# Kernel tuning notes

Measured on AMD Instinct MI355X. Metric: run time of the kernel, lower is better.

Reference implementation:

```python
import jax, jax.numpy as jnp
import numpy as np

NODE = 112
L1, L2, L3 = 256, 128, 64
BATCH = 2048


def setup_inputs() -> dict:
    key = jax.random.key(0)
    ks = jax.random.split(key, 19)
    def n(k, shape, s=0.05):
        return jax.random.normal(k, shape, jnp.float32) * s
    return {
        "x": jax.random.uniform(ks[0], (BATCH, NODE, NODE), jnp.float32),
        # GAT1: proj Linear(112->L1); attention Linear(2*L1->1) split into (wa1, wb1, ba1)
        "Wp1": n(ks[1], (L1, NODE)), "bp1": n(ks[2], (L1,)),
        "wa1": n(ks[3], (L1,)), "wb1": n(ks[4], (L1,)), "ba1": n(ks[5], ()),
        # Pool1: proj Linear(L1->1)
        "Wpool1": n(ks[6], (L1,)), "bpool1": n(ks[7], ()),
        # GAT2
        "Wp2": n(ks[8], (L2, L1)), "bp2": n(ks[9], (L2,)),
        "wa2": n(ks[10], (L2,)), "wb2": n(ks[11], (L2,)), "ba2": n(ks[12], ()),
        # Pool2
        "Wpool2": n(ks[13], (L2,)), "bpool2": n(ks[14], ()),
        # FC head
        "Wfc1": n(ks[15], (L3, L2)), "bfc1": n(ks[16], (L3,)),
        "Wfc2": n(ks[17], (1, L3)), "bfc2": n(ks[18], (1,)),
    }


def _gat(a, h, Wp, bp, wa, wb, ba):
    # h: [B,N,Din] -> [B,N,O]
    h = jnp.einsum('bnd,od->bno', h, Wp) + bp
    # attention(concat(h_i, h_j)) == h_i.wa + h_j.wb + ba (linear over concat splits)
    s = jnp.einsum('bno,o->bn', h, wa)  # first-half contribution
    t = jnp.einsum('bno,o->bn', h, wb)  # second-half contribution
    e = jax.nn.relu(s[:, :, None] + t[:, None, :] + ba)  # [B,N,N]
    att = jnp.exp(e) * a
    att = att / jnp.sum(att, axis=-1, keepdims=True)
    return jnp.einsum('bij,bjo->bio', att, h) + h


def _pool(adj, hidden, w, b, k):
    scores = jax.nn.sigmoid(jnp.einsum('bnd,d->bn', hidden, w) + b)  # [B,N]
    vals, idx = jax.lax.top_k(scores, k)  # sorted descending, like torch.topk
    hidden = jnp.take_along_axis(hidden, idx[:, :, None], axis=1) * vals[:, :, None]
    adj = jnp.take_along_axis(adj, idx[:, :, None], axis=1)
    adj = jnp.take_along_axis(adj, idx[:, None, :], axis=2)
    adj = adj / jnp.sum(adj, axis=-1, keepdims=True)
    return adj, hidden


def reference(x, Wp1, bp1, wa1, wb1, ba1, Wpool1, bpool1,
              Wp2, bp2, wa2, wb2, ba2, Wpool2, bpool2,
              Wfc1, bfc1, Wfc2, bfc2):
    b = x.shape[0]
    h = jnp.broadcast_to(jnp.eye(NODE, dtype=x.dtype), (b, NODE, NODE))
    h = jax.nn.relu(_gat(x, h, Wp1, bp1, wa1, wb1, ba1))
    k1 = max(2, int(0.5 * NODE))          # 56
    a, h = _pool(x, h, Wpool1, bpool1, k1)
    h = jax.nn.relu(_gat(a, h, Wp2, bp2, wa2, wb2, ba2))
    k2 = max(2, int(0.5 * k1))            # 28
    a, h = _pool(a, h, Wpool2, bpool2, k2)
    h = jnp.mean(h, axis=1)               # [B,L2]
    h = jax.nn.relu(h @ Wfc1.T + bfc1)
    return h @ Wfc2.T + bfc2              # [B,1]
```

## Files before the change

kernel.cpp:

```cpp
#include <hip/hip_runtime.h>

#define NODE 112
#define KP1 56
#define KP2 28
#define D1 256
#define D2 128
#define NBATCH 2048
#define NCH 4
#define CR 28
#define WR 7

typedef const float* __restrict__ fp;

__global__ void k0a(fp Wp1, fp bp1, fp wa1, fp wb1,
                    float* __restrict__ s1, float* __restrict__ t1)
{
    int tid = threadIdx.x;
    if (tid < NODE) {
        float sa = 0.f, sb = 0.f;
        for (int o = 0; o < D1; o++) {
            float h = Wp1[o*NODE + tid] + bp1[o];
            sa += h * wa1[o];
            sb += h * wb1[o];
        }
        s1[tid] = sa; t1[tid] = sb;
    }
}

__global__ void k0b(fp Wp1, fp bp1, fp ba1, fp Wp2,
                    const float* __restrict__ s1, const float* __restrict__ t1,
                    float* __restrict__ hp, float* __restrict__ E1, float* __restrict__ W2T)
{
    int g = blockIdx.x*blockDim.x + threadIdx.x;
    int stride = gridDim.x*blockDim.x;
    for (int e = g; e < NODE*D1; e += stride) {
        int j = e >> 8, o = e & 255;
        hp[e] = Wp1[o*NODE + j] + bp1[o];
    }
    float ba = ba1[0];
    for (int e = g; e < NODE*NODE; e += stride) {
        int i = e / NODE, j = e - i*NODE;
        E1[e] = expf(fmaxf(s1[i] + t1[j] + ba, 0.f));
    }
    for (int e = g; e < D1*D2; e += stride) {
        int d = e >> 7, o = e & 127;
        W2T[e] = Wp2[o*D1 + d];
    }
}

__device__ __forceinline__ void topk_wave(volatile float* sc, int n, int k,
                                          int* idxo, float* valo, int tid)
{
    for (int it = 0; it < k; it++) {
        float v = (tid < n) ? sc[tid] : -1e30f;
        int bi = tid;
        int j2 = tid + 64;
        if (j2 < n) { float v2 = sc[j2]; if (v2 > v) { v = v2; bi = j2; } }
        #pragma unroll
        for (int off = 32; off; off >>= 1) {
            float ov = __shfl_xor(v, off, 64);
            int   oi = __shfl_xor(bi, off, 64);
            if (ov > v || (ov == v && oi < bi)) { v = ov; bi = oi; }
        }
        if (tid == 0) { idxo[it] = bi; valo[it] = v; sc[bi] = -1e30f; }
    }
}

__device__ __forceinline__ float sigm(float v) { return 1.f/(1.f + expf(-v)); }

__global__ __launch_bounds__(256, 2) void gnn_fast(
    fp x, fp Wpool1, fp bpool1, fp bp2, fp wa2, fp wb2, fp ba2,
    fp Wpool2, fp bpool2, fp Wfc1, fp bfc1, fp Wfc2, fp bfc2,
    fp hp, fp E1, fp W2T, float* __restrict__ out)
{
    __shared__ __align__(16) float hg[KP1*D1];
    __shared__ __align__(16) float awc[CR*NODE];
    __shared__ float rinv[CR];
    __shared__ float sc1[NODE];
    __shared__ int   idx1[KP1];
    __shared__ float vals1[KP1];
    __shared__ int   sel[NODE];
    __shared__ float s2v[KP1], t2v[KP1];
    __shared__ float rs2inv[KP1];
    __shared__ float sc2[KP1];
    __shared__ int   idx2[KP2];
    __shared__ float vals2[KP2];
    __shared__ float hmean[D2];

    const int tid = threadIdx.x;
    const int lane = tid & 63, wave = tid >> 6;
    const int b = blockIdx.x;
    const float* xb = x + (size_t)b*NODE*NODE;

    const float4 wp1v = *(const float4*)(Wpool1 + 4*lane);
    const float bpool1v = bpool1[0];

    float h1r[NCH][WR][4];

    #pragma unroll
    for (int c = 0; c < NCH; c++) {
        const int i0 = c*CR;
        {
            int rloc = tid >> 3, seg = tid & 7;
            float ps = 0.f;
            if (rloc < CR) {
                int i = i0 + rloc;
                const float2* Erow = (const float2*)(E1 + i*NODE + seg*14);
                const float2* xrow = (const float2*)(xb + i*NODE + seg*14);
                float2* arow = (float2*)(awc + rloc*NODE + seg*14);
                #pragma unroll
                for (int q = 0; q < 7; q++) {
                    float2 ev = Erow[q], xv = xrow[q];
                    float2 v = make_float2(ev.x*xv.x, ev.y*xv.y);
                    arow[q] = v;
                    ps += v.x + v.y;
                }
            }
            ps += __shfl_xor(ps, 1, 64);
            ps += __shfl_xor(ps, 2, 64);
            ps += __shfl_xor(ps, 4, 64);
            if (rloc < CR && seg == 0) rinv[rloc] = 1.f/ps;
        }
        __syncthreads();

        float acc[WR][4];
        #pragma unroll
        for (int r = 0; r < WR; r++) { acc[r][0]=0.f; acc[r][1]=0.f; acc[r][2]=0.f; acc[r][3]=0.f; }
        const int r0 = wave*WR;
        for (int jq = 0; jq < NODE/4; jq++) {
            const int j = jq*4;
            float4 hv0 = *(const float4*)(hp + (j+0)*D1 + 4*lane);
            float4 hv1 = *(const float4*)(hp + (j+1)*D1 + 4*lane);
            float4 hv2 = *(const float4*)(hp + (j+2)*D1 + 4*lane);
            float4 hv3 = *(const float4*)(hp + (j+3)*D1 + 4*lane);
            #pragma unroll
            for (int r = 0; r < WR; r++) {
                float4 a4 = *(const float4*)&awc[(r0+r)*NODE + j];
                acc[r][0] += a4.x*hv0.x + a4.y*hv1.x + a4.z*hv2.x + a4.w*hv3.x;
                acc[r][1] += a4.x*hv0.y + a4.y*hv1.y + a4.z*hv2.y + a4.w*hv3.y;
                acc[r][2] += a4.x*hv0.z + a4.y*hv1.z + a4.z*hv2.z + a4.w*hv3.z;
                acc[r][3] += a4.x*hv0.w + a4.y*hv1.w + a4.z*hv2.w + a4.w*hv3.w;
            }
        }
        #pragma unroll
        for (int r = 0; r < WR; r++) {
            const int i = i0 + r0 + r;
            float ri = rinv[r0 + r];
            float4 hpi = *(const float4*)(hp + i*D1 + 4*lane);
            float v0 = fmaxf(acc[r][0]*ri + hpi.x, 0.f);
            float v1 = fmaxf(acc[r][1]*ri + hpi.y, 0.f);
            float v2 = fmaxf(acc[r][2]*ri + hpi.z, 0.f);
            float v3 = fmaxf(acc[r][3]*ri + hpi.w, 0.f);
            h1r[c][r][0]=v0; h1r[c][r][1]=v1; h1r[c][r][2]=v2; h1r[c][r][3]=v3;
            float p = v0*wp1v.x + v1*wp1v.y + v2*wp1v.z + v3*wp1v.w;
            #pragma unroll
            for (int off = 32; off; off >>= 1) p += __shfl_xor(p, off, 64);
            if (lane == 0) sc1[i] = sigm(p + bpool1v);
        }
        __syncthreads();
    }

    if (tid < 64) topk_wave(sc1, NODE, KP1, idx1, vals1, tid);
    __syncthreads();
    if (tid < NODE) sel[tid] = -1;
    __syncthreads();
    if (tid < KP1) sel[idx1[tid]] = tid;
    __syncthreads();

    #pragma unroll
    for (int c = 0; c < NCH; c++) {
        #pragma unroll
        for (int r = 0; r < WR; r++) {
            int i = c*CR + wave*WR + r;
            int k = sel[i];
            if (k >= 0) {
                float vs = vals1[k];
                float4 v = make_float4(h1r[c][r][0]*vs, h1r[c][r][1]*vs,
                                       h1r[c][r][2]*vs, h1r[c][r][3]*vs);
                *(float4*)&hg[k*D1 + 4*lane] = v;
            }
        }
    }
    __syncthreads();

    {
        const int g = tid >> 5;
        const int cs = tid & 31;
        float acc2[WR][4];
        #pragma unroll
        for (int r = 0; r < WR; r++) { acc2[r][0]=0.f; acc2[r][1]=0.f; acc2[r][2]=0.f; acc2[r][3]=0.f; }
        for (int dq = 0; dq < D1/4; dq++) {
            const int d = dq*4;
            float4 w0 = *(const float4*)(W2T + (d+0)*D2 + 4*cs);
            float4 w1 = *(const float4*)(W2T + (d+1)*D2 + 4*cs);
            float4 w2 = *(const float4*)(W2T + (d+2)*D2 + 4*cs);
            float4 w3 = *(const float4*)(W2T + (d+3)*D2 + 4*cs);
            #pragma unroll
            for (int r = 0; r < WR; r++) {
                float4 a4 = *(const float4*)&hg[(g*WR+r)*D1 + d];
                acc2[r][0] += a4.x*w0.x + a4.y*w1.x + a4.z*w2.x + a4.w*w3.x;
                acc2[r][1] += a4.x*w0.y + a4.y*w1.y + a4.z*w2.y + a4.w*w3.y;
                acc2[r][2] += a4.x*w0.z + a4.y*w1.z + a4.z*w2.z + a4.w*w3.z;
                acc2[r][3] += a4.x*w0.w + a4.y*w1.w + a4.z*w2.w + a4.w*w3.w;
            }
        }
        float4 b2 = *(const float4*)(bp2 + 4*cs);
        __syncthreads();
        #pragma unroll
        for (int r = 0; r < WR; r++) {
            *(float4*)&hg[(g*WR+r)*D1 + 4*cs] =
                make_float4(acc2[r][0]+b2.x, acc2[r][1]+b2.y, acc2[r][2]+b2.z, acc2[r][3]+b2.w);
        }
    }
    __syncthreads();

    if (tid < 4*KP1) {
        int row = tid >> 2, seg = tid & 3;
        float sa = 0.f, sb = 0.f;
        #pragma unroll
        for (int q = 0; q < 8; q++) {
            float4 hv = *(const float4*)&hg[row*D1 + seg*32 + q*4];
            float4 va = *(const float4*)(wa2 + seg*32 + q*4);
            float4 vb = *(const float4*)(wb2 + seg*32 + q*4);
            sa += hv.x*va.x + hv.y*va.y + hv.z*va.z + hv.w*va.w;
            sb += hv.x*vb.x + hv.y*vb.y + hv.z*vb.z + hv.w*vb.w;
        }
        sa += __shfl_xor(sa, 1, 64); sa += __shfl_xor(sa, 2, 64);
        sb += __shfl_xor(sb, 1, 64); sb += __shfl_xor(sb, 2, 64);
        if (seg == 0) { s2v[row] = sa; t2v[row] = sb; }
    }
    __syncthreads();

    if (tid < 4*KP1) {
        int rloc = tid >> 2, seg = tid & 3;
        float ps = 0.f;
        int gi = idx1[rloc];
        float srow = s2v[rloc];
        const float ba2v = ba2[0];
        const float* xrow = xb + gi*NODE;
        float* arow = awc + rloc*KP1 + seg*14;
        #pragma unroll
        for (int q = 0; q < 14; q++) {
            int j = seg*14 + q;
            float e = fmaxf(srow + t2v[j] + ba2v, 0.f);
            float v = expf(e) * xrow[idx1[j]];
            arow[q] = v;
            ps += v;
        }
        ps += __shfl_xor(ps, 1, 64); ps += __shfl_xor(ps, 2, 64);
        if (seg == 0) rs2inv[rloc] = 1.f/ps;
    }
    __syncthreads();

    {
        const int g = tid >> 5, cs = tid & 31;
        float acc3[WR][4];
        #pragma unroll
        for (int r = 0; r < WR; r++) { acc3[r][0]=0.f; acc3[r][1]=0.f; acc3[r][2]=0.f; acc3[r][3]=0.f; }
        for (int lq = 0; lq < KP1/4; lq++) {
            const int l = lq*4;
            float4 p0 = *(const float4*)&hg[(l+0)*D1 + 4*cs];
            float4 p1 = *(const float4*)&hg[(l+1)*D1 + 4*cs];
            float4 p2 = *(const float4*)&hg[(l+2)*D1 + 4*cs];
            float4 p3 = *(const float4*)&hg[(l+3)*D1 + 4*cs];
            #pragma unroll
            for (int r = 0; r < WR; r++) {
                float4 a4 = *(const float4*)&awc[(g*WR+r)*KP1 + l];
                acc3[r][0] += a4.x*p0.x + a4.y*p1.x + a4.z*p2.x + a4.w*p3.x;
                acc3[r][1] += a4.x*p0.y + a4.y*p1.y + a4.z*p2.y + a4.w*p3.y;
                acc3[r][2] += a4.x*p0.z + a4.y*p1.z + a4.z*p2.z + a4.w*p3.z;
                acc3[r][3] += a4.x*p0.w + a4.y*p1.w + a4.z*p2.w + a4.w*p3.w;
            }
        }
        const float4 wp2v = *(const float4*)(Wpool2 + 4*cs);
        const float bpool2v = bpool2[0];
        #pragma unroll
        for (int r = 0; r < WR; r++) {
            int row = g*WR + r;
            float ri = rs2inv[row];
            float4 hpj = *(const float4*)&hg[row*D1 + 4*cs];
            float v0 = fmaxf(acc3[r][0]*ri + hpj.x, 0.f);
            float v1 = fmaxf(acc3[r][1]*ri + hpj.y, 0.f);
            float v2 = fmaxf(acc3[r][2]*ri + hpj.z, 0.f);
            float v3 = fmaxf(acc3[r][3]*ri + hpj.w, 0.f);
            *(float4*)&hg[row*D1 + D2 + 4*cs] = make_float4(v0, v1, v2, v3);
            float p = v0*wp2v.x + v1*wp2v.y + v2*wp2v.z + v3*wp2v.w;
            p += __shfl_xor(p, 16, 64); p += __shfl_xor(p, 8, 64);
            p += __shfl_xor(p, 4, 64);  p += __shfl_xor(p, 2, 64);
            p += __shfl_xor(p, 1, 64);
            if (cs == 0) sc2[row] = sigm(p + bpool2v);
        }
    }
    __syncthreads();

    if (tid < 64) topk_wave(sc2, KP1, KP2, idx2, vals2, tid);
    __syncthreads();

    if (tid < D2) {
        float m = 0.f;
        for (int k = 0; k < KP2; k++) m += hg[idx2[k]*D1 + D2 + tid] * vals2[k];
        hmean[tid] = m * (1.f/28.f);
    }
    __syncthreads();

    if (tid < 64) {
        float s = 0.f;
        #pragma unroll
        for (int q = 0; q < 32; q++) {
            float4 w = *(const float4*)(Wfc1 + tid*D2 + q*4);
            s += hmean[q*4+0]*w.x + hmean[q*4+1]*w.y + hmean[q*4+2]*w.z + hmean[q*4+3]*w.w;
        }
        s = fmaxf(s + bfc1[tid], 0.f);
        float v = s * Wfc2[tid];
        #pragma unroll
        for (int off = 32; off; off >>= 1) v += __shfl_xor(v, off, 64);
        if (tid == 0) out[b] = v + bfc2[0];
    }
}

__global__ __launch_bounds__(256) void gnn_fallback(
    fp x, fp Wp1, fp bp1, fp wa1, fp wb1, fp ba1,
    fp Wpool1, fp bpool1, fp Wp2, fp bp2, fp wa2, fp wb2, fp ba2,
    fp Wpool2, fp bpool2, fp Wfc1, fp bfc1, fp Wfc2, fp bfc2,
    float* __restrict__ out)
{
    __shared__ __align__(16) float hg[KP1*D1];
    __shared__ __align__(16) float awc[CR*NODE];
    __shared__ float s1v[NODE], t1v[NODE];
    __shared__ float sc1[NODE];
    __shared__ float rsc[KP1];
    __shared__ float redc[4*CR];
    __shared__ int   idx1[KP1];
    __shared__ float vals1[KP1];
    __shared__ float s2v[KP1], t2v[KP1];
    __shared__ float sc2[KP1];
    __shared__ int   idx2[KP2];
    __shared__ float vals2[KP2];
    __shared__ float hmean[D2];

    const int tid = threadIdx.x;
    const int lane = tid & 63, wave = tid >> 6;
    const int b = blockIdx.x;
    const float* xb = x + (size_t)b*NODE*NODE;

    const float wpool1v = Wpool1[tid];
    const float bpool1v = bpool1[0];
    const float ba1v    = ba1[0];
    const float* wrow = Wp1 + tid*NODE;
    const float bp1v = bp1[tid];

    if (tid < NODE) {
        float sa = 0.f, sb = 0.f;
        for (int o = 0; o < D1; o++) {
            float h = Wp1[o*NODE + tid] + bp1[o];
            sa += h * wa1[o];
            sb += h * wb1[o];
        }
        s1v[tid] = sa; t1v[tid] = sb;
    }
    __syncthreads();

    for (int c = 0; c < NODE/CR; c++) {
        const int i0 = c*CR;
        for (int e = tid; e < CR*NODE; e += 256) {
            int r = e / NODE, j = e - r*NODE;
            int i = i0 + r;
            float ee = fmaxf(s1v[i] + t1v[j] + ba1v, 0.f);
            awc[e] = expf(ee) * xb[i*NODE + j];
        }
        __syncthreads();
        if (tid < CR) {
            float s = 0.f;
            for (int j = 0; j < NODE; j++) s += awc[tid*NODE + j];
            rsc[tid] = s;
        }
        __syncthreads();
        float acc[CR];
        #pragma unroll
        for (int r = 0; r < CR; r++) acc[r] = 0.f;
        for (int jg = 0; jg < NODE/4; jg++) {
            float4 w = *(const float4*)(wrow + jg*4);
            float h0 = w.x + bp1v, h1 = w.y + bp1v, h2 = w.z + bp1v, h3 = w.w + bp1v;
            #pragma unroll
            for (int r = 0; r < CR; r++) {
                float4 a4 = *(const float4*)&awc[r*NODE + jg*4];
                acc[r] += a4.x*h0 + a4.y*h1 + a4.z*h2 + a4.w*h3;
            }
        }
        float part[CR];
        #pragma unroll
        for (int r = 0; r < CR; r++) {
            float hpi = wrow[i0 + r] + bp1v;
            float h1v = fmaxf(acc[r]/rsc[r] + hpi, 0.f);
            part[r] = h1v * wpool1v;
        }
        #pragma unroll
        for (int r = 0; r < CR; r++) {
            float v = part[r];
            #pragma unroll
            for (int off = 32; off; off >>= 1) v += __shfl_xor(v, off, 64);
            if (lane == 0) redc[wave*CR + r] = v;
        }
        __syncthreads();
        if (tid < CR) {
            float s = redc[tid] + redc[CR+tid] + redc[2*CR+tid] + redc[3*CR+tid];
            sc1[i0 + tid] = sigm(s + bpool1v);
        }
        __syncthreads();
    }

    if (tid < 64) topk_wave(sc1, NODE, KP1, idx1, vals1, tid);
    __syncthreads();

    for (int c = 0; c < KP1/CR; c++) {
        const int k0 = c*CR;
        for (int e = tid; e < CR*NODE; e += 256) {
            int r = e / NODE, j = e - r*NODE;
            int i = idx1[k0 + r];
            float ee = fmaxf(s1v[i] + t1v[j] + ba1v, 0.f);
            awc[e] = expf(ee) * xb[i*NODE + j];
        }
        __syncthreads();
        if (tid < CR) {
            float s = 0.f;
            for (int j = 0; j < NODE; j++) s += awc[tid*NODE + j];
            rsc[tid] = s;
        }
        __syncthreads();
        float acc[CR];
        #pragma unroll
        for (int r = 0; r < CR; r++) acc[r] = 0.f;
        for (int jg = 0; jg < NODE/4; jg++) {
            float4 w = *(const float4*)(wrow + jg*4);
            float h0 = w.x + bp1v, h1 = w.y + bp1v, h2 = w.z + bp1v, h3 = w.w + bp1v;
            #pragma unroll
            for (int r = 0; r < CR; r++) {
                float4 a4 = *(const float4*)&awc[r*NODE + jg*4];
                acc[r] += a4.x*h0 + a4.y*h1 + a4.z*h2 + a4.w*h3;
            }
        }
        #pragma unroll
        for (int r = 0; r < CR; r++) {
            int k = k0 + r;
            float hpi = wrow[idx1[k]] + bp1v;
            float h1v = fmaxf(acc[r]/rsc[r] + hpi, 0.f);
            hg[k*D1 + tid] = h1v * vals1[k];
        }
        __syncthreads();
    }

    {
        const int half = tid >> 7, o = tid & 127;
        const float* w2row = Wp2 + o*D1;
        float acc2[CR];
        #pragma unroll
        for (int r = 0; r < CR; r++) acc2[r] = 0.f;
        for (int d4 = 0; d4 < D1; d4 += 4) {
            float4 w = *(const float4*)(w2row + d4);
            #pragma unroll
            for (int r = 0; r < CR; r++) {
                float4 h4 = *(const float4*)&hg[(half*CR + r)*D1 + d4];
                acc2[r] += h4.x*w.x + h4.y*w.y + h4.z*w.z + h4.w*w.w;
            }
        }
        __syncthreads();
        float bp2v = bp2[o];
        #pragma unroll
        for (int r = 0; r < CR; r++)
            hg[(half*CR + r)*D1 + o] = acc2[r] + bp2v;
    }
    __syncthreads();

    if (tid < KP1) {
        float sa = 0.f, sb = 0.f;
        for (int o2 = 0; o2 < D2; o2++) {
            float hv = hg[tid*D1 + o2];
            sa += hv * wa2[o2];
            sb += hv * wb2[o2];
        }
        s2v[tid] = sa; t2v[tid] = sb;
    }
    __syncthreads();

    {
        const float ba2v = ba2[0];
        for (int e = tid; e < KP1*KP1; e += 256) {
            int i = e / KP1, j = e - i*KP1;
            float ee = fmaxf(s2v[i] + t2v[j] + ba2v, 0.f);
            awc[e] = expf(ee) * xb[idx1[i]*NODE + idx1[j]];
        }
    }
    __syncthreads();
    if (tid < KP1) {
        float s = 0.f;
        for (int j = 0; j < KP1; j++) s += awc[tid*KP1 + j];
        rsc[tid] = s;
    }
    __syncthreads();

    {
        const int half = tid >> 7, o = tid & 127;
        float acc3[CR];
        #pragma unroll
        for (int r = 0; r < CR; r++) acc3[r] = 0.f;
        for (int l4 = 0; l4 < KP1; l4 += 4) {
            float p0 = hg[(l4+0)*D1 + o];
            float p1 = hg[(l4+1)*D1 + o];
            float p2 = hg[(l4+2)*D1 + o];
            float p3 = hg[(l4+3)*D1 + o];
            #pragma unroll
            for (int r = 0; r < CR; r++) {
                float4 a4 = *(const float4*)&awc[(half*CR + r)*KP1 + l4];
                acc3[r] += a4.x*p0 + a4.y*p1 + a4.z*p2 + a4.w*p3;
            }
        }
        const float wpool2v = Wpool2[o];
        float part2[CR];
        #pragma unroll
        for (int r = 0; r < CR; r++) {
            int n = half*CR + r;
            float h2v = fmaxf(acc3[r]/rsc[n] + hg[n*D1 + o], 0.f);
            hg[n*D1 + D2 + o] = h2v;
            part2[r] = h2v * wpool2v;
        }
        #pragma unroll
        for (int r = 0; r < CR; r++) {
            float v = part2[r];
            #pragma unroll
            for (int off = 32; off; off >>= 1) v += __shfl_xor(v, off, 64);
            if (lane == 0) redc[wave*CR + r] = v;
        }
    }
    __syncthreads();
    {
        const float bpool2v = bpool2[0];
        if (tid < KP1) {
            int hh = tid / CR, rr = tid - hh*CR;
            float s = redc[(2*hh)*CR + rr] + redc[(2*hh+1)*CR + rr];
            sc2[tid] = sigm(s + bpool2v);
        }
    }
    __syncthreads();

    if (tid < 64) topk_wave(sc2, KP1, KP2, idx2, vals2, tid);
    __syncthreads();

    if (tid < D2) {
        float m = 0.f;
        for (int k = 0; k < KP2; k++) m += hg[idx2[k]*D1 + D2 + tid] * vals2[k];
        hmean[tid] = m * (1.f/28.f);
    }
    __syncthreads();

    if (tid < 64) {
        float s = 0.f;
        for (int d = 0; d < D2; d++) s += hmean[d] * Wfc1[tid*D2 + d];
        s = fmaxf(s + bfc1[tid], 0.f);
        float v = s * Wfc2[tid];
        #pragma unroll
        for (int off = 32; off; off >>= 1) v += __shfl_xor(v, off, 64);
        if (tid == 0) out[b] = v + bfc2[0];
    }
}

extern "C" void kernel_launch(void* const* d_in, const int* in_sizes, int n_in,
                              void* d_out, int out_size, void* d_ws, size_t ws_size,
                              hipStream_t stream) {
    (void)in_sizes; (void)n_in; (void)out_size;
    fp x      = (fp)d_in[0];
    fp Wp1    = (fp)d_in[1];
    fp bp1    = (fp)d_in[2];
    fp wa1    = (fp)d_in[3];
    fp wb1    = (fp)d_in[4];
    fp ba1    = (fp)d_in[5];
    fp Wpool1 = (fp)d_in[6];
    fp bpool1 = (fp)d_in[7];
    fp Wp2    = (fp)d_in[8];
    fp bp2    = (fp)d_in[9];
    fp wa2    = (fp)d_in[10];
    fp wb2    = (fp)d_in[11];
    fp ba2    = (fp)d_in[12];
    fp Wpool2 = (fp)d_in[13];
    fp bpool2 = (fp)d_in[14];
    fp Wfc1   = (fp)d_in[15];
    fp bfc1   = (fp)d_in[16];
    fp Wfc2   = (fp)d_in[17];
    fp bfc2   = (fp)d_in[18];

    const size_t WS_NEED = (size_t)(NODE*D1 + NODE*NODE + D1*D2 + 2*NODE) * sizeof(float);

    if (ws_size >= WS_NEED) {
        float* hp  = (float*)d_ws;
        float* E1  = hp  + NODE*D1;
        float* W2T = E1  + NODE*NODE;
        float* s1  = W2T + D1*D2;
        float* t1  = s1  + NODE;
        hipLaunchKernelGGL(k0a, dim3(1), dim3(256), 0, stream,
                           Wp1, bp1, wa1, wb1, s1, t1);
        hipLaunchKernelGGL(k0b, dim3(64), dim3(256), 0, stream,
                           Wp1, bp1, ba1, Wp2, s1, t1, hp, E1, W2T);
        hipLaunchKernelGGL(gnn_fast, dim3(NBATCH), dim3(256), 0, stream,
                           x, Wpool1, bpool1, bp2, wa2, wb2, ba2,
                           Wpool2, bpool2, Wfc1, bfc1, Wfc2, bfc2,
                           hp, E1, W2T, (float*)d_out);
    } else {
        hipLaunchKernelGGL(gnn_fallback, dim3(NBATCH), dim3(256), 0, stream,
                           x, Wp1, bp1, wa1, wb1, ba1, Wpool1, bpool1,
                           Wp2, bp2, wa2, wb2, ba2, Wpool2, bpool2,
                           Wfc1, bfc1, Wfc2, bfc2, (float*)d_out);
    }
}
```

Baseline: 762.9 us.

## Compute full GAT1 attention in one pass with aliased shared buffer

Replaces the four-chunk GAT1 loop with a single pass. The full 112x112 attention matrix is built in shared memory, aliased with the hg buffer, and each wave accumulates 28 rows over all of hp. This cuts the hp global reloads from four passes to one and removes the per-chunk barriers. It also splits the k0a reduction across thread pairs and overlaps the sel init with top-k. The cost is 112 accumulator floats per thread, which greatly raises register pressure under launch_bounds(256,2) and risks spills.

```diff
diff --git a/kernel.cpp b/kernel.cpp
--- a/kernel.cpp
+++ b/kernel.cpp
@@ -6,9 +6,9 @@
 #define D1 256
 #define D2 128
 #define NBATCH 2048
-#define NCH 4
+#define RW 28
+#define GR 7
 #define CR 28
-#define WR 7
 
 typedef const float* __restrict__ fp;
 
@@ -16,15 +16,18 @@
                     float* __restrict__ s1, float* __restrict__ t1)
 {
     int tid = threadIdx.x;
-    if (tid < NODE) {
-        float sa = 0.f, sb = 0.f;
-        for (int o = 0; o < D1; o++) {
-            float h = Wp1[o*NODE + tid] + bp1[o];
+    int i = tid >> 1, half = tid & 1;
+    float sa = 0.f, sb = 0.f;
+    if (i < NODE) {
+        for (int o = half*128; o < half*128 + 128; o++) {
+            float h = Wp1[o*NODE + i] + bp1[o];
             sa += h * wa1[o];
             sb += h * wb1[o];
         }
-        s1[tid] = sa; t1[tid] = sb;
-    }
+    }
+    sa += __shfl_xor(sa, 1, 64);
+    sb += __shfl_xor(sb, 1, 64);
+    if (i < NODE && half == 0) { s1[i] = sa; t1[i] = sb; }
 }
 
 __global__ void k0b(fp Wp1, fp bp1, fp ba1, fp Wp2,
@@ -73,9 +76,9 @@
     fp Wpool2, fp bpool2, fp Wfc1, fp bfc1, fp Wfc2, fp bfc2,
     fp hp, fp E1, fp W2T, float* __restrict__ out)
 {
-    __shared__ __align__(16) float hg[KP1*D1];
-    __shared__ __align__(16) float awc[CR*NODE];
-    __shared__ float rinv[CR];
+    __shared__ __align__(16) float ovl[KP1*D1];
+    __shared__ __align__(16) float awc2[KP1*KP1];
+    __shared__ float rinv[NODE];
     __shared__ float sc1[NODE];
     __shared__ int   idx1[KP1];
     __shared__ float vals1[KP1];
@@ -87,6 +90,9 @@
     __shared__ float vals2[KP2];
     __shared__ float hmean[D2];
 
+    float* awcF = ovl;
+    float* hg   = ovl;
+
     const int tid = threadIdx.x;
     const int lane = tid & 63, wave = tid >> 6;
     const int b = blockIdx.x;
@@ -95,90 +101,82 @@
     const float4 wp1v = *(const float4*)(Wpool1 + 4*lane);
     const float bpool1v = bpool1[0];
 
-    float h1r[NCH][WR][4];
-
-    #pragma unroll
-    for (int c = 0; c < NCH; c++) {
-        const int i0 = c*CR;
-        {
-            int rloc = tid >> 3, seg = tid & 7;
+    {
+        const int seg = tid & 3;
+        #pragma unroll
+        for (int pass = 0; pass < 2; pass++) {
+            const int i = (tid >> 2) + pass*64;
             float ps = 0.f;
-            if (rloc < CR) {
-                int i = i0 + rloc;
-                const float2* Erow = (const float2*)(E1 + i*NODE + seg*14);
-                const float2* xrow = (const float2*)(xb + i*NODE + seg*14);
-                float2* arow = (float2*)(awc + rloc*NODE + seg*14);
+            if (i < NODE) {
+                const float4* Er = (const float4*)(E1 + i*NODE + seg*28);
+                const float4* xr = (const float4*)(xb + i*NODE + seg*28);
+                float4* ar = (float4*)(awcF + i*NODE + seg*28);
                 #pragma unroll
                 for (int q = 0; q < 7; q++) {
-                    float2 ev = Erow[q], xv = xrow[q];
-                    float2 v = make_float2(ev.x*xv.x, ev.y*xv.y);
-                    arow[q] = v;
-                    ps += v.x + v.y;
+                    float4 e = Er[q], xv = xr[q];
+                    float4 v = make_float4(e.x*xv.x, e.y*xv.y, e.z*xv.z, e.w*xv.w);
+                    ar[q] = v;
+                    ps += (v.x + v.y) + (v.z + v.w);
                 }
             }
             ps += __shfl_xor(ps, 1, 64);
             ps += __shfl_xor(ps, 2, 64);
-            ps += __shfl_xor(ps, 4, 64);
-            if (rloc < CR && seg == 0) rinv[rloc] = 1.f/ps;
-        }
-        __syncthreads();
-
-        float acc[WR][4];
-        #pragma unroll
-        for (int r = 0; r < WR; r++) { acc[r][0]=0.f; acc[r][1]=0.f; acc[r][2]=0.f; acc[r][3]=0.f; }
-        const int r0 = wave*WR;
-        for (int jq = 0; jq < NODE/4; jq++) {
-            const int j = jq*4;
-            float4 hv0 = *(const float4*)(hp + (j+0)*D1 + 4*lane);
-            float4 hv1 = *(const float4*)(hp + (j+1)*D1 + 4*lane);
-            float4 hv2 = *(const float4*)(hp + (j+2)*D1 + 4*lane);
-            float4 hv3 = *(const float4*)(hp + (j+3)*D1 + 4*lane);
-            #pragma unroll
-            for (int r = 0; r < WR; r++) {
-                float4 a4 = *(const float4*)&awc[(r0+r)*NODE + j];
-                acc[r][0] += a4.x*hv0.x + a4.y*hv1.x + a4.z*hv2.x + a4.w*hv3.x;
-                acc[r][1] += a4.x*hv0.y + a4.y*hv1.y + a4.z*hv2.y + a4.w*hv3.y;
-                acc[r][2] += a4.x*hv0.z + a4.y*hv1.z + a4.z*hv2.z + a4.w*hv3.z;
-                acc[r][3] += a4.x*hv0.w + a4.y*hv1.w + a4.z*hv2.w + a4.w*hv3.w;
-            }
-        }
-        #pragma unroll
-        for (int r = 0; r < WR; r++) {
-            const int i = i0 + r0 + r;
-            float ri = rinv[r0 + r];
-            float4 hpi = *(const float4*)(hp + i*D1 + 4*lane);
-            float v0 = fmaxf(acc[r][0]*ri + hpi.x, 0.f);
-            float v1 = fmaxf(acc[r][1]*ri + hpi.y, 0.f);
-            float v2 = fmaxf(acc[r][2]*ri + hpi.z, 0.f);
-            float v3 = fmaxf(acc[r][3]*ri + hpi.w, 0.f);
-            h1r[c][r][0]=v0; h1r[c][r][1]=v1; h1r[c][r][2]=v2; h1r[c][r][3]=v3;
-            float p = v0*wp1v.x + v1*wp1v.y + v2*wp1v.z + v3*wp1v.w;
-            #pragma unroll
-            for (int off = 32; off; off >>= 1) p += __shfl_xor(p, off, 64);
-            if (lane == 0) sc1[i] = sigm(p + bpool1v);
-        }
-        __syncthreads();
-    }
+            if (i < NODE && seg == 0) rinv[i] = 1.f/ps;
+        }
+    }
+    __syncthreads();
+
+    const int r0 = wave*RW;
+    float acc[RW][4];
+    #pragma unroll
+    for (int r = 0; r < RW; r++) { acc[r][0]=0.f; acc[r][1]=0.f; acc[r][2]=0.f; acc[r][3]=0.f; }
+    #pragma unroll 2
+    for (int jq = 0; jq < NODE/4; jq++) {
+        const int j = jq*4;
+        float4 hv0 = *(const float4*)(hp + (j+0)*D1 + 4*lane);
+        float4 hv1 = *(const float4*)(hp + (j+1)*D1 + 4*lane);
+        float4 hv2 = *(const float4*)(hp + (j+2)*D1 + 4*lane);
+        float4 hv3 = *(const float4*)(hp + (j+3)*D1 + 4*lane);
+        #pragma unroll
+        for (int r = 0; r < RW; r++) {
+            float4 a4 = *(const float4*)&awcF[(r0+r)*NODE + j];
+            acc[r][0] += a4.x*hv0.x + a4.y*hv1.x + a4.z*hv2.x + a4.w*hv3.x;
+            acc[r][1] += a4.x*hv0.y + a4.y*hv1.y + a4.z*hv2.y + a4.w*hv3.y;
+            acc[r][2] += a4.x*hv0.z + a4.y*hv1.z + a4.z*hv2.z + a4.w*hv3.z;
+            acc[r][3] += a4.x*hv0.w + a4.y*hv1.w + a4.z*hv2.w + a4.w*hv3.w;
+        }
+    }
+    #pragma unroll
+    for (int r = 0; r < RW; r++) {
+        const int i = r0 + r;
+        const float ri = rinv[i];
+        float4 hpi = *(const float4*)(hp + i*D1 + 4*lane);
+        float v0 = fmaxf(acc[r][0]*ri + hpi.x, 0.f);
+        float v1 = fmaxf(acc[r][1]*ri + hpi.y, 0.f);
+        float v2 = fmaxf(acc[r][2]*ri + hpi.z, 0.f);
+        float v3 = fmaxf(acc[r][3]*ri + hpi.w, 0.f);
+        acc[r][0]=v0; acc[r][1]=v1; acc[r][2]=v2; acc[r][3]=v3;
+        float p = v0*wp1v.x + v1*wp1v.y + v2*wp1v.z + v3*wp1v.w;
+        #pragma unroll
+        for (int off = 32; off; off >>= 1) p += __shfl_xor(p, off, 64);
+        if (lane == 0) sc1[i] = sigm(p + bpool1v);
+    }
+    __syncthreads();
 
     if (tid < 64) topk_wave(sc1, NODE, KP1, idx1, vals1, tid);
-    __syncthreads();
-    if (tid < NODE) sel[tid] = -1;
+    else if (tid >= 128 && tid < 128 + NODE) sel[tid - 128] = -1;
     __syncthreads();
     if (tid < KP1) sel[idx1[tid]] = tid;
     __syncthreads();
 
     #pragma unroll
-    for (int c = 0; c < NCH; c++) {
-        #pragma unroll
-        for (int r = 0; r < WR; r++) {
-            int i = c*CR + wave*WR + r;
-            int k = sel[i];
-            if (k >= 0) {
-                float vs = vals1[k];
-                float4 v = make_float4(h1r[c][r][0]*vs, h1r[c][r][1]*vs,
-                                       h1r[c][r][2]*vs, h1r[c][r][3]*vs);
-                *(float4*)&hg[k*D1 + 4*lane] = v;
-            }
+    for (int r = 0; r < RW; r++) {
+        const int i = r0 + r;
+        const int k = sel[i];
+        if (k >= 0) {
+            const float vs = vals1[k];
+            *(float4*)&hg[k*D1 + 4*lane] =
+                make_float4(acc[r][0]*vs, acc[r][1]*vs, acc[r][2]*vs, acc[r][3]*vs);
         }
     }
     __syncthreads();
@@ -186,9 +184,10 @@
     {
         const int g = tid >> 5;
         const int cs = tid & 31;
-        float acc2[WR][4];
-        #pragma unroll
-        for (int r = 0; r < WR; r++) { acc2[r][0]=0.f; acc2[r][1]=0.f; acc2[r][2]=0.f; acc2[r][3]=0.f; }
+        float acc2[GR][4];
+        #pragma unroll
+        for (int r = 0; r < GR; r++) { acc2[r][0]=0.f; acc2[r][1]=0.f; acc2[r][2]=0.f; acc2[r][3]=0.f; }
+        #pragma unroll 2
         for (int dq = 0; dq < D1/4; dq++) {
             const int d = dq*4;
             float4 w0 = *(const float4*)(W2T + (d+0)*D2 + 4*cs);
@@ -196,8 +195,8 @@
             float4 w2 = *(const float4*)(W2T + (d+2)*D2 + 4*cs);
             float4 w3 = *(const float4*)(W2T + (d+3)*D2 + 4*cs);
             #pragma unroll
-            for (int r = 0; r < WR; r++) {
-                float4 a4 = *(const float4*)&hg[(g*WR+r)*D1 + d];
+            for (int r = 0; r < GR; r++) {
+                float4 a4 = *(const float4*)&hg[(g*GR+r)*D1 + d];
                 acc2[r][0] += a4.x*w0.x + a4.y*w1.x + a4.z*w2.x + a4.w*w3.x;
                 acc2[r][1] += a4.x*w0.y + a4.y*w1.y + a4.z*w2.y + a4.w*w3.y;
                 acc2[r][2] += a4.x*w0.z + a4.y*w1.z + a4.z*w2.z + a4.w*w3.z;
@@ -207,8 +206,8 @@
         float4 b2 = *(const float4*)(bp2 + 4*cs);
         __syncthreads();
         #pragma unroll
-        for (int r = 0; r < WR; r++) {
-            *(float4*)&hg[(g*WR+r)*D1 + 4*cs] =
+        for (int r = 0; r < GR; r++) {
+            *(float4*)&hg[(g*GR+r)*D1 + 4*cs] =
                 make_float4(acc2[r][0]+b2.x, acc2[r][1]+b2.y, acc2[r][2]+b2.z, acc2[r][3]+b2.w);
         }
     }
@@ -238,7 +237,7 @@
         float srow = s2v[rloc];
         const float ba2v = ba2[0];
         const float* xrow = xb + gi*NODE;
-        float* arow = awc + rloc*KP1 + seg*14;
+        float* arow = awc2 + rloc*KP1 + seg*14;
         #pragma unroll
         for (int q = 0; q < 14; q++) {
             int j = seg*14 + q;
@@ -254,9 +253,10 @@
 
     {
         const int g = tid >> 5, cs = tid & 31;
-        float acc3[WR][4];
-        #pragma unroll
-        for (int r = 0; r < WR; r++) { acc3[r][0]=0.f; acc3[r][1]=0.f; acc3[r][2]=0.f; acc3[r][3]=0.f; }
+        float acc3[GR][4];
+        #pragma unroll
+        for (int r = 0; r < GR; r++) { acc3[r][0]=0.f; acc3[r][1]=0.f; acc3[r][2]=0.f; acc3[r][3]=0.f; }
+        #pragma unroll 2
         for (int lq = 0; lq < KP1/4; lq++) {
             const int l = lq*4;
             float4 p0 = *(const float4*)&hg[(l+0)*D1 + 4*cs];
@@ -264,8 +264,8 @@
             float4 p2 = *(const float4*)&hg[(l+2)*D1 + 4*cs];
             float4 p3 = *(const float4*)&hg[(l+3)*D1 + 4*cs];
             #pragma unroll
-            for (int r = 0; r < WR; r++) {
-                float4 a4 = *(const float4*)&awc[(g*WR+r)*KP1 + l];
+            for (int r = 0; r < GR; r++) {
+                float4 a4 = *(const float4*)&awc2[(g*GR+r)*KP1 + l];
                 acc3[r][0] += a4.x*p0.x + a4.y*p1.x + a4.z*p2.x + a4.w*p3.x;
                 acc3[r][1] += a4.x*p0.y + a4.y*p1.y + a4.z*p2.y + a4.w*p3.y;
                 acc3[r][2] += a4.x*p0.z + a4.y*p1.z + a4.z*p2.z + a4.w*p3.z;
@@ -275,8 +275,8 @@
         const float4 wp2v = *(const float4*)(Wpool2 + 4*cs);
         const float bpool2v = bpool2[0];
         #pragma unroll
-        for (int r = 0; r < WR; r++) {
-            int row = g*WR + r;
+        for (int r = 0; r < GR; r++) {
+            int row = g*GR + r;
             float ri = rs2inv[row];
             float4 hpj = *(const float4*)&hg[row*D1 + 4*cs];
             float v0 = fmaxf(acc3[r][0]*ri + hpj.x, 0.f);
```

Result: slower. 1.406 ms (+84.2%).
